# Optimization experiments

Hardware: AMD Instinct MI355X
Metric: run time of the kernel (lower is better)

The kernel has to match this reference:

```python
import jax, jax.numpy as jnp
import numpy as np

N, D, K = 65536, 64, 1024
BB, HH, WW = 64, 32, 32


def setup_inputs() -> dict:
    key = jax.random.key(0)
    k1, k2 = jax.random.split(key)
    x = jax.random.normal(k1, (N, D), dtype=jnp.float32)
    # embedding initialized uniform(-1/K, 1/K)
    weight = jax.random.uniform(k2, (K, D), dtype=jnp.float32, minval=-1.0 / K, maxval=1.0 / K)
    return {"x": x, "weight": weight, "B": BB, "H": HH, "W": WW}


def reference(x, weight, B, H, W):
    beta = 1.0
    # pairwise squared distances [N, K]
    distances = (jnp.sum(x ** 2, axis=1, keepdims=True)
                 + jnp.sum(weight ** 2, axis=1)
                 - 2.0 * x @ weight.T)
    encoding_indices = jnp.argmin(distances, axis=1)  # [N]
    # one-hot @ weight is just a gather
    quantized = weight[encoding_indices]  # [N, D]
    e_latent_loss = jnp.mean((jax.lax.stop_gradient(quantized) - x) ** 2)
    q_latent_loss = jnp.mean((jax.lax.stop_gradient(x) - quantized) ** 2)
    loss = q_latent_loss + beta * e_latent_loss
    # straight-through estimator
    quantized = x + jax.lax.stop_gradient(quantized - x)
    quantized = quantized.reshape(B, H, W, D).transpose(0, 3, 1, 2)  # [B, D, H, W]
    return loss, quantized, encoding_indices[:, None]
```

## Files before the change

### kernel.cpp

```cpp
#include <hip/hip_runtime.h>

#define N_ROWS 65536
#define DIM 64
#define KCB 1024
#define Q_ELEMS 4194304
#define RPB 128
#define KQ 256
#define TILE 64
#define NTILES 4


__device__ __forceinline__ float np_pairwise_sumsq64(const float* v) {
#pragma clang fp contract(off)
    float r[8];
#pragma unroll
    for (int j = 0; j < 8; ++j) r[j] = v[j] * v[j];
#pragma unroll
    for (int i = 8; i < 64; i += 8) {
#pragma unroll
        for (int j = 0; j < 8; ++j) {
            float s = v[i + j] * v[i + j];
            r[j] = r[j] + s;
        }
    }
    return ((r[0] + r[1]) + (r[2] + r[3])) + ((r[4] + r[5]) + (r[6] + r[7]));
}

__global__ void wnorm_kernel(const float* __restrict__ w, float* __restrict__ wn2) {
    int k = blockIdx.x * 256 + threadIdx.x;
    if (k >= KCB) return;
    wn2[k] = np_pairwise_sumsq64(w + (size_t)k * DIM);
}

__global__ __launch_bounds__(256, 2) void vq_kernel(const float* __restrict__ x,
                                                    const float* __restrict__ w,
                                                    const float* __restrict__ wn2,
                                                    float* __restrict__ out,
                                                    float* __restrict__ partial) {
    __shared__ float wtile[4][TILE * DIM];

    const int t = threadIdx.x;
    const int lane = t & 63;
    const int wv = t >> 6;
    const int rowbase = blockIdx.x * RPB;
    const int r0 = rowbase + lane;
    const int r1 = r0 + 64;

    float xr0[DIM], xr1[DIM];
    const float4* xv0 = (const float4*)(x + (size_t)r0 * DIM);
    const float4* xv1 = (const float4*)(x + (size_t)r1 * DIM);
#pragma unroll
    for (int i = 0; i < 16; ++i) {
        float4 a = xv0[i];
        xr0[4 * i + 0] = a.x; xr0[4 * i + 1] = a.y; xr0[4 * i + 2] = a.z; xr0[4 * i + 3] = a.w;
        float4 b = xv1[i];
        xr1[4 * i + 0] = b.x; xr1[4 * i + 1] = b.y; xr1[4 * i + 2] = b.z; xr1[4 * i + 3] = b.w;
    }
    const float S0 = np_pairwise_sumsq64(xr0);
    const float S1 = np_pairwise_sumsq64(xr1);

    const int kbase = wv * KQ;
    float best0 = 3.4e38f, best1 = 3.4e38f;
    int bi0 = 0, bi1 = 0;

    for (int tile = 0; tile < NTILES; ++tile) {
        const float* gsrc = w + (size_t)(kbase + tile * TILE) * DIM;
        float* ldst = &wtile[wv][0];
#pragma unroll
        for (int j = 0; j < 16; ++j) {
            float4 v = *(const float4*)(gsrc + j * 256 + lane * 4);
            *(float4*)(ldst + j * 256 + lane * 4) = v;
        }

        for (int c = 0; c < TILE; c += 4) {
            const float* w0 = ldst + c * DIM;
            float a00 = 0.f, a01 = 0.f, a02 = 0.f, a03 = 0.f;
            float a10 = 0.f, a11 = 0.f, a12 = 0.f, a13 = 0.f;
#pragma unroll
            for (int d = 0; d < DIM; d += 4) {
                float4 u0 = *(const float4*)(w0 + 0 * DIM + d);
                float4 u1 = *(const float4*)(w0 + 1 * DIM + d);
                float4 u2 = *(const float4*)(w0 + 2 * DIM + d);
                float4 u3 = *(const float4*)(w0 + 3 * DIM + d);
                float p0 = xr0[d], p1 = xr0[d + 1], p2 = xr0[d + 2], p3 = xr0[d + 3];
                float q0 = xr1[d], q1 = xr1[d + 1], q2 = xr1[d + 2], q3 = xr1[d + 3];
                a00 = __builtin_fmaf(p0, u0.x, a00); a00 = __builtin_fmaf(p1, u0.y, a00);
                a00 = __builtin_fmaf(p2, u0.z, a00); a00 = __builtin_fmaf(p3, u0.w, a00);
                a01 = __builtin_fmaf(p0, u1.x, a01); a01 = __builtin_fmaf(p1, u1.y, a01);
                a01 = __builtin_fmaf(p2, u1.z, a01); a01 = __builtin_fmaf(p3, u1.w, a01);
                a02 = __builtin_fmaf(p0, u2.x, a02); a02 = __builtin_fmaf(p1, u2.y, a02);
                a02 = __builtin_fmaf(p2, u2.z, a02); a02 = __builtin_fmaf(p3, u2.w, a02);
                a03 = __builtin_fmaf(p0, u3.x, a03); a03 = __builtin_fmaf(p1, u3.y, a03);
                a03 = __builtin_fmaf(p2, u3.z, a03); a03 = __builtin_fmaf(p3, u3.w, a03);
                a10 = __builtin_fmaf(q0, u0.x, a10); a10 = __builtin_fmaf(q1, u0.y, a10);
                a10 = __builtin_fmaf(q2, u0.z, a10); a10 = __builtin_fmaf(q3, u0.w, a10);
                a11 = __builtin_fmaf(q0, u1.x, a11); a11 = __builtin_fmaf(q1, u1.y, a11);
                a11 = __builtin_fmaf(q2, u1.z, a11); a11 = __builtin_fmaf(q3, u1.w, a11);
                a12 = __builtin_fmaf(q0, u2.x, a12); a12 = __builtin_fmaf(q1, u2.y, a12);
                a12 = __builtin_fmaf(q2, u2.z, a12); a12 = __builtin_fmaf(q3, u2.w, a12);
                a13 = __builtin_fmaf(q0, u3.x, a13); a13 = __builtin_fmaf(q1, u3.y, a13);
                a13 = __builtin_fmaf(q2, u3.z, a13); a13 = __builtin_fmaf(q3, u3.w, a13);
            }
            const int k = kbase + tile * TILE + c;
            float wnA = wn2[k + 0], wnB = wn2[k + 1], wnC = wn2[k + 2], wnD = wn2[k + 3];
            float d00 = (S0 + wnA) - 2.0f * a00;
            float d01 = (S0 + wnB) - 2.0f * a01;
            float d02 = (S0 + wnC) - 2.0f * a02;
            float d03 = (S0 + wnD) - 2.0f * a03;
            if (d00 < best0) { best0 = d00; bi0 = k + 0; }
            if (d01 < best0) { best0 = d01; bi0 = k + 1; }
            if (d02 < best0) { best0 = d02; bi0 = k + 2; }
            if (d03 < best0) { best0 = d03; bi0 = k + 3; }
            float d10 = (S1 + wnA) - 2.0f * a10;
            float d11 = (S1 + wnB) - 2.0f * a11;
            float d12 = (S1 + wnC) - 2.0f * a12;
            float d13 = (S1 + wnD) - 2.0f * a13;
            if (d10 < best1) { best1 = d10; bi1 = k + 0; }
            if (d11 < best1) { best1 = d11; bi1 = k + 1; }
            if (d12 < best1) { best1 = d12; bi1 = k + 2; }
            if (d13 < best1) { best1 = d13; bi1 = k + 3; }
        }
    }

    __syncthreads();
    float* cbd = (float*)&wtile[0][0];
    int*   cbk = (int*)((char*)&wtile[0][0] + 2048);
    float* red = (float*)((char*)&wtile[0][0] + 4096);
    cbd[wv * 128 + lane]      = best0;  cbk[wv * 128 + lane]      = bi0;
    cbd[wv * 128 + 64 + lane] = best1;  cbk[wv * 128 + 64 + lane] = bi1;
    __syncthreads();

    float lsum = 0.f;
    if (t < 128) {
        const int rb = t;
        float bd = cbd[0 * 128 + rb]; int bk = cbk[0 * 128 + rb];
#pragma unroll
        for (int q = 1; q < 4; ++q) {
            float dq = cbd[q * 128 + rb]; int kq = cbk[q * 128 + rb];
            if (dq < bd) { bd = dq; bk = kq; }
        }
        float xcur[DIM];
        if (wv == 0) {
#pragma unroll
            for (int d = 0; d < DIM; ++d) xcur[d] = xr0[d];
        } else {
#pragma unroll
            for (int d = 0; d < DIM; ++d) xcur[d] = xr1[d];
        }
        const int n = rowbase + rb;
        const int b = n >> 10;
        const int hw = n & 1023;
        float* outq = out + 1 + (size_t)b * 65536 + hw;
        const float4* wr4 = (const float4*)(w + (size_t)bk * DIM);
#pragma unroll
        for (int i = 0; i < 16; ++i) {
            float4 u = wr4[i];
            float d0 = u.x - xcur[4 * i + 0];
            float d1 = u.y - xcur[4 * i + 1];
            float d2 = u.z - xcur[4 * i + 2];
            float d3 = u.w - xcur[4 * i + 3];
            lsum += d0 * d0; lsum += d1 * d1; lsum += d2 * d2; lsum += d3 * d3;
            outq[(size_t)(4 * i + 0) * 1024] = xcur[4 * i + 0] + d0;
            outq[(size_t)(4 * i + 1) * 1024] = xcur[4 * i + 1] + d1;
            outq[(size_t)(4 * i + 2) * 1024] = xcur[4 * i + 2] + d2;
            outq[(size_t)(4 * i + 3) * 1024] = xcur[4 * i + 3] + d3;
        }
        out[1 + Q_ELEMS + n] = (float)bk;
    }
#pragma unroll
    for (int off = 32; off > 0; off >>= 1) lsum += __shfl_down(lsum, off, 64);
    if (lane == 0) red[wv] = lsum;
    __syncthreads();
    if (t == 0) partial[blockIdx.x] = (red[0] + red[1]) + (red[2] + red[3]);
}

__global__ void finish_kernel(const float* __restrict__ partial, float* __restrict__ out) {
    float v = partial[threadIdx.x] + partial[threadIdx.x + 256];
#pragma unroll
    for (int off = 32; off > 0; off >>= 1) v += __shfl_down(v, off, 64);
    __shared__ float red[4];
    const int lane = threadIdx.x & 63;
    const int wv = threadIdx.x >> 6;
    if (lane == 0) red[wv] = v;
    __syncthreads();
    if (threadIdx.x == 0) {
        float total = (red[0] + red[1]) + (red[2] + red[3]);
        out[0] = total * (2.0f / (float)(N_ROWS * DIM));
    }
}

extern "C" void kernel_launch(void* const* d_in, const int* in_sizes, int n_in,
                              void* d_out, int out_size, void* d_ws, size_t ws_size,
                              hipStream_t stream) {
    const float* x = (const float*)d_in[0];
    const float* w = (const float*)d_in[1];
    float* out = (float*)d_out;

    char* ws = (char*)d_ws;
    float* wn2 = (float*)(ws + 0);
    float* partial = (float*)(ws + 4096);

    wnorm_kernel<<<4, 256, 0, stream>>>(w, wn2);
    vq_kernel<<<N_ROWS / RPB, 256, 0, stream>>>(x, w, wn2, out, partial);
    finish_kernel<<<1, 256, 0, stream>>>(partial, out);
}
```

Before: 211.2 us.

## Read codebook rows via wave-uniform scalar loads instead of LDS tiles

Drops the LDS staging of codebook tiles. Each wave now reads its codebook rows straight from global memory, with the wave index made uniform through readfirstlane so those loads can become scalar loads. The inner loop is simplified to one codebook row at a time with two accumulators, and the occupancy hint is raised from 2 to 3 blocks per SIMD. The aim is to remove the LDS traffic and its bandwidth limit, at the cost of less instruction-level parallelism per iteration and a dependence on scalar cache throughput.

```diff
diff --git a/kernel.cpp b/kernel.cpp
--- a/kernel.cpp
+++ b/kernel.cpp
@@ -6,8 +6,6 @@
 #define Q_ELEMS 4194304
 #define RPB 128
 #define KQ 256
-#define TILE 64
-#define NTILES 4
 
 
 __device__ __forceinline__ float np_pairwise_sumsq64(const float* v) {
@@ -32,16 +30,14 @@
     wn2[k] = np_pairwise_sumsq64(w + (size_t)k * DIM);
 }
 
-__global__ __launch_bounds__(256, 2) void vq_kernel(const float* __restrict__ x,
+__global__ __launch_bounds__(256, 3) void vq_kernel(const float* __restrict__ x,
                                                     const float* __restrict__ w,
                                                     const float* __restrict__ wn2,
                                                     float* __restrict__ out,
                                                     float* __restrict__ partial) {
-    __shared__ float wtile[4][TILE * DIM];
-
     const int t = threadIdx.x;
     const int lane = t & 63;
-    const int wv = t >> 6;
+    const int wv = __builtin_amdgcn_readfirstlane(t >> 6);
     const int rowbase = blockIdx.x * RPB;
     const int r0 = rowbase + lane;
     const int r1 = r0 + 64;
@@ -60,83 +56,42 @@
     const float S1 = np_pairwise_sumsq64(xr1);
 
     const int kbase = wv * KQ;
+    const float* __restrict__ wq = w + (size_t)kbase * DIM;
     float best0 = 3.4e38f, best1 = 3.4e38f;
-    int bi0 = 0, bi1 = 0;
+    int bi0 = kbase, bi1 = kbase;
 
-    for (int tile = 0; tile < NTILES; ++tile) {
-        const float* gsrc = w + (size_t)(kbase + tile * TILE) * DIM;
-        float* ldst = &wtile[wv][0];
+#pragma unroll 1
+    for (int c = 0; c < KQ; ++c) {
+        const float* wr = wq + c * DIM;
+        float a0 = 0.f, a1 = 0.f;
 #pragma unroll
-        for (int j = 0; j < 16; ++j) {
-            float4 v = *(const float4*)(gsrc + j * 256 + lane * 4);
-            *(float4*)(ldst + j * 256 + lane * 4) = v;
+        for (int d = 0; d < DIM; ++d) {
+            float wd = wr[d];
+            a0 = __builtin_fmaf(xr0[d], wd, a0);
+            a1 = __builtin_fmaf(xr1[d], wd, a1);
         }
-
-        for (int c = 0; c < TILE; c += 4) {
-            const float* w0 = ldst + c * DIM;
-            float a00 = 0.f, a01 = 0.f, a02 = 0.f, a03 = 0.f;
-            float a10 = 0.f, a11 = 0.f, a12 = 0.f, a13 = 0.f;
-#pragma unroll
-            for (int d = 0; d < DIM; d += 4) {
-                float4 u0 = *(const float4*)(w0 + 0 * DIM + d);
-                float4 u1 = *(const float4*)(w0 + 1 * DIM + d);
-                float4 u2 = *(const float4*)(w0 + 2 * DIM + d);
-                float4 u3 = *(const float4*)(w0 + 3 * DIM + d);
-                float p0 = xr0[d], p1 = xr0[d + 1], p2 = xr0[d + 2], p3 = xr0[d + 3];
-                float q0 = xr1[d], q1 = xr1[d + 1], q2 = xr1[d + 2], q3 = xr1[d + 3];
-                a00 = __builtin_fmaf(p0, u0.x, a00); a00 = __builtin_fmaf(p1, u0.y, a00);
-                a00 = __builtin_fmaf(p2, u0.z, a00); a00 = __builtin_fmaf(p3, u0.w, a00);
-                a01 = __builtin_fmaf(p0, u1.x, a01); a01 = __builtin_fmaf(p1, u1.y, a01);
-                a01 = __builtin_fmaf(p2, u1.z, a01); a01 = __builtin_fmaf(p3, u1.w, a01);
-                a02 = __builtin_fmaf(p0, u2.x, a02); a02 = __builtin_fmaf(p1, u2.y, a02);
-                a02 = __builtin_fmaf(p2, u2.z, a02); a02 = __builtin_fmaf(p3, u2.w, a02);
-                a03 = __builtin_fmaf(p0, u3.x, a03); a03 = __builtin_fmaf(p1, u3.y, a03);
-                a03 = __builtin_fmaf(p2, u3.z, a03); a03 = __builtin_fmaf(p3, u3.w, a03);
-                a10 = __builtin_fmaf(q0, u0.x, a10); a10 = __builtin_fmaf(q1, u0.y, a10);
-                a10 = __builtin_fmaf(q2, u0.z, a10); a10 = __builtin_fmaf(q3, u0.w, a10);
-                a11 = __builtin_fmaf(q0, u1.x, a11); a11 = __builtin_fmaf(q1, u1.y, a11);
-                a11 = __builtin_fmaf(q2, u1.z, a11); a11 = __builtin_fmaf(q3, u1.w, a11);
-                a12 = __builtin_fmaf(q0, u2.x, a12); a12 = __builtin_fmaf(q1, u2.y, a12);
-                a12 = __builtin_fmaf(q2, u2.z, a12); a12 = __builtin_fmaf(q3, u2.w, a12);
-                a13 = __builtin_fmaf(q0, u3.x, a13); a13 = __builtin_fmaf(q1, u3.y, a13);
-                a13 = __builtin_fmaf(q2, u3.z, a13); a13 = __builtin_fmaf(q3, u3.w, a13);
-            }
-            const int k = kbase + tile * TILE + c;
-            float wnA = wn2[k + 0], wnB = wn2[k + 1], wnC = wn2[k + 2], wnD = wn2[k + 3];
-            float d00 = (S0 + wnA) - 2.0f * a00;
-            float d01 = (S0 + wnB) - 2.0f * a01;
-            float d02 = (S0 + wnC) - 2.0f * a02;
-            float d03 = (S0 + wnD) - 2.0f * a03;
-            if (d00 < best0) { best0 = d00; bi0 = k + 0; }
-            if (d01 < best0) { best0 = d01; bi0 = k + 1; }
-            if (d02 < best0) { best0 = d02; bi0 = k + 2; }
-            if (d03 < best0) { best0 = d03; bi0 = k + 3; }
-            float d10 = (S1 + wnA) - 2.0f * a10;
-            float d11 = (S1 + wnB) - 2.0f * a11;
-            float d12 = (S1 + wnC) - 2.0f * a12;
-            float d13 = (S1 + wnD) - 2.0f * a13;
-            if (d10 < best1) { best1 = d10; bi1 = k + 0; }
-            if (d11 < best1) { best1 = d11; bi1 = k + 1; }
-            if (d12 < best1) { best1 = d12; bi1 = k + 2; }
-            if (d13 < best1) { best1 = d13; bi1 = k + 3; }
-        }
+        const int k = kbase + c;
+        const float wnk = wn2[k];
+        float d0 = (S0 + wnk) - 2.0f * a0;
+        float d1 = (S1 + wnk) - 2.0f * a1;
+        if (d0 < best0) { best0 = d0; bi0 = k; }
+        if (d1 < best1) { best1 = d1; bi1 = k; }
     }
 
-    __syncthreads();
-    float* cbd = (float*)&wtile[0][0];
-    int*   cbk = (int*)((char*)&wtile[0][0] + 2048);
-    float* red = (float*)((char*)&wtile[0][0] + 4096);
-    cbd[wv * 128 + lane]      = best0;  cbk[wv * 128 + lane]      = bi0;
-    cbd[wv * 128 + 64 + lane] = best1;  cbk[wv * 128 + 64 + lane] = bi1;
+    __shared__ float cbd[4][RPB];
+    __shared__ int   cbk[4][RPB];
+    __shared__ float red[4];
+    cbd[wv][lane]      = best0;  cbk[wv][lane]      = bi0;
+    cbd[wv][64 + lane] = best1;  cbk[wv][64 + lane] = bi1;
     __syncthreads();
 
     float lsum = 0.f;
     if (t < 128) {
         const int rb = t;
-        float bd = cbd[0 * 128 + rb]; int bk = cbk[0 * 128 + rb];
+        float bd = cbd[0][rb]; int bk = cbk[0][rb];
 #pragma unroll
         for (int q = 1; q < 4; ++q) {
-            float dq = cbd[q * 128 + rb]; int kq = cbk[q * 128 + rb];
+            float dq = cbd[q][rb]; int kq = cbk[q][rb];
             if (dq < bd) { bd = dq; bk = kq; }
         }
         float xcur[DIM];
```

Measured after the change: 312.3 us. 1.48x slower.
